# Kernel tuning notes

Hardware: AMD Instinct MI355X
Metric: run time of the kernel (lower is better)

The kernel has to match this reference:

```python
import jax, jax.numpy as jnp
import numpy as np

N = 100000
D = 64
H = 4 * D  # 256
E = 1000000


def setup_inputs() -> dict:
    key = jax.random.key(0)
    ks = jax.random.split(key, 9)
    return {
        "loc_feat": jax.random.normal(ks[0], (N, D), dtype=jnp.float32),
        "geo_src": jax.random.randint(ks[1], (E,), 0, N),
        "geo_dst": jax.random.randint(ks[2], (E,), 0, N),
        "trans_src": jax.random.randint(ks[3], (E,), 0, N),
        "trans_dst": jax.random.randint(ks[4], (E,), 0, N),
        "trans_w": jax.random.uniform(ks[5], (E,), dtype=jnp.float32),
        "W1": jax.random.normal(ks[6], (D, H), dtype=jnp.float32) * (1.0 / np.sqrt(D)),
        "b1": jax.random.normal(ks[7], (H,), dtype=jnp.float32) * 0.01,
        "W2": jax.random.normal(ks[8], (H, 1), dtype=jnp.float32) * (1.0 / np.sqrt(H)),
    }


def reference(loc_feat, geo_src, geo_dst, trans_src, trans_dst, trans_w, W1, b1, W2):
    n = loc_feat.shape[0]
    # etype 'geo': copy_u + mean  -> segment mean of src features at dst
    geo_sum = jax.ops.segment_sum(loc_feat[geo_src], geo_dst, num_segments=n)
    cnt = jax.ops.segment_sum(jnp.ones(geo_src.shape[0], loc_feat.dtype), geo_dst, num_segments=n)
    geo = jnp.where(cnt[:, None] > 0, geo_sum / jnp.maximum(cnt, 1.0)[:, None], 0.0)
    # etype 'trans': u_mul_e + sum -> weighted segment sum
    trans = jax.ops.segment_sum(loc_feat[trans_src] * trans_w[:, None], trans_dst, num_segments=n)
    # semantic attention fuse over the two relation views
    z = jnp.stack([geo, trans], axis=1)          # [N, 2, D]
    h = jnp.tanh(jnp.einsum('nkd,dh->nkh', z, W1) + b1)  # [N, 2, H]
    w = jnp.einsum('nkh,ho->nko', h, W2).mean(0)  # [2, 1] (mean over nodes)
    beta = jax.nn.softmax(w, axis=0)              # [2, 1]
    return (beta[None, :, :] * z).sum(1)          # [N, D]
```

## Files before the change

kernel.cpp:

```cpp
#include <hip/hip_runtime.h>
#include <hip/hip_bf16.h>

#define N_NODES 100000
#define DIM 64
#define HID 256
#define E_EDGES 1000000
#define TWO_N (2 * N_NODES)
#define MLP_ROWBLOCKS (TWO_N / 64)

#define TILE 240
#define NBINS 417
#define CAP 3072
#define EPB 4096
#define GEO_BLOCKS 245

typedef short short8 __attribute__((ext_vector_type(8)));
typedef float f32x4 __attribute__((ext_vector_type(4)));

__device__ __forceinline__ float tanh_fast(float x) {
    x = fminf(fmaxf(x, -15.0f), 15.0f);
    float e = __expf(2.0f * x);
    return (e - 1.0f) / (e + 1.0f);
}

__device__ __forceinline__ unsigned short f2bf(float x) {
    unsigned u = __float_as_uint(x);
    u = u + 0x7FFFu + ((u >> 16) & 1u);
    return (unsigned short)(u >> 16);
}

__global__ void bin_fill_kernel(const int* __restrict__ gs, const int* __restrict__ gd,
                                const int* __restrict__ ts, const int* __restrict__ td,
                                const float* __restrict__ tw,
                                int* __restrict__ gcount,
                                int* __restrict__ gbin, int2* __restrict__ tbin) {
    __shared__ int hist[NBINS];
    __shared__ int baseS[NBINS];
    __shared__ int cur[NBINS];
    int t = threadIdx.x;
    int blk = blockIdx.x;
    int rel = (blk >= GEO_BLOCKS) ? 1 : 0;
    int e0 = (rel ? blk - GEO_BLOCKS : blk) * EPB;
    const int* dstp = rel ? td : gd;

    for (int i = t; i < NBINS; i += 256) { hist[i] = 0; cur[i] = 0; }
    __syncthreads();

    #pragma unroll
    for (int j = 0; j < EPB / 256; ++j) {
        int e = e0 + j * 256 + t;
        if (e < E_EDGES) atomicAdd(&hist[dstp[e] / TILE], 1);
    }
    __syncthreads();

    for (int i = t; i < NBINS; i += 256) {
        int h = hist[i];
        baseS[i] = (h > 0) ? (i * CAP + atomicAdd(&gcount[rel * NBINS + i], h)) : 0;
    }
    __syncthreads();

    if (!rel) {
        #pragma unroll
        for (int j = 0; j < EPB / 256; ++j) {
            int e = e0 + j * 256 + t;
            if (e < E_EDGES) {
                int d = dstp[e];
                int bin = d / TILE;
                int pos = atomicAdd(&cur[bin], 1);
                int idx = baseS[bin] + pos;
                if (idx < (bin + 1) * CAP)
                    gbin[idx] = gs[e] | ((d - bin * TILE) << 20);
            }
        }
    } else {
        #pragma unroll
        for (int j = 0; j < EPB / 256; ++j) {
            int e = e0 + j * 256 + t;
            if (e < E_EDGES) {
                int d = dstp[e];
                int bin = d / TILE;
                int pos = atomicAdd(&cur[bin], 1);
                int idx = baseS[bin] + pos;
                if (idx < (bin + 1) * CAP)
                    tbin[idx] = make_int2(ts[e] | ((d - bin * TILE) << 20),
                                          __float_as_int(tw[e]));
            }
        }
    }
}

__global__ void __launch_bounds__(512) aggregate_kernel(
        const float* __restrict__ feat,
        const int* __restrict__ gbin, const int2* __restrict__ tbin,
        const int* __restrict__ gcount,
        float* __restrict__ out_geo, float* __restrict__ trans_out,
        int* __restrict__ cnt_out) {
    __shared__ int   srcS[CAP];
    __shared__ float wS[CAP];
    __shared__ int   histS[TILE];
    __shared__ int   baseS[TILE];
    __shared__ int   curS[TILE];
    __shared__ int   scanS[256];

    int b = blockIdx.x;
    int rel = (b >= NBINS) ? 1 : 0;
    int bin = rel ? b - NBINS : b;
    int node0 = bin * TILE;
    int nNodes = min(TILE, N_NODES - node0);
    int t = threadIdx.x, lane = t & 63, wave = t >> 6;

    int nE = gcount[b];
    if (nE > CAP) nE = CAP;

    for (int i = t; i < TILE; i += 512) histS[i] = 0;
    __syncthreads();

    if (!rel) {
        const int* bp = gbin + (size_t)bin * CAP;
        for (int i = t; i < nE; i += 512) atomicAdd(&histS[bp[i] >> 20], 1);
    } else {
        const int2* bp = tbin + (size_t)bin * CAP;
        for (int i = t; i < nE; i += 512) atomicAdd(&histS[bp[i].x >> 20], 1);
    }
    __syncthreads();

    if (t < 256) scanS[t] = (t < TILE) ? histS[t] : 0;
    __syncthreads();
    #pragma unroll
    for (int off = 1; off < 256; off <<= 1) {
        int add = 0;
        if (t < 256 && t >= off) add = scanS[t - off];
        __syncthreads();
        if (t < 256) scanS[t] += add;
        __syncthreads();
    }
    if (t < TILE) {
        int base = scanS[t] - histS[t];
        baseS[t] = base;
        curS[t] = base;
    }
    __syncthreads();

    if (!rel) {
        const int* bp = gbin + (size_t)bin * CAP;
        for (int i = t; i < nE; i += 512) {
            int p = bp[i];
            int pos = atomicAdd(&curS[p >> 20], 1);
            srcS[pos] = p & 0xFFFFF;
        }
    } else {
        const int2* bp = tbin + (size_t)bin * CAP;
        for (int i = t; i < nE; i += 512) {
            int2 p = bp[i];
            int pos = atomicAdd(&curS[p.x >> 20], 1);
            srcS[pos] = p.x & 0xFFFFF;
            wS[pos] = __int_as_float(p.y);
        }
    }
    __syncthreads();

    for (int nl = wave; nl < nNodes; nl += 8) {
        int deg = histS[nl];
        int base = baseS[nl];
        float acc = 0.0f;
        if (!rel) {
            int k = 0;
            for (; k + 3 < deg; k += 4) {
                int s0 = srcS[base + k], s1 = srcS[base + k + 1];
                int s2 = srcS[base + k + 2], s3 = srcS[base + k + 3];
                float v0 = feat[(size_t)s0 * DIM + lane];
                float v1 = feat[(size_t)s1 * DIM + lane];
                float v2 = feat[(size_t)s2 * DIM + lane];
                float v3 = feat[(size_t)s3 * DIM + lane];
                acc += (v0 + v1) + (v2 + v3);
            }
            for (; k < deg; ++k) acc += feat[(size_t)srcS[base + k] * DIM + lane];
            out_geo[(size_t)(node0 + nl) * DIM + lane] = acc;
        } else {
            int k = 0;
            for (; k + 3 < deg; k += 4) {
                int s0 = srcS[base + k], s1 = srcS[base + k + 1];
                int s2 = srcS[base + k + 2], s3 = srcS[base + k + 3];
                float w0 = wS[base + k], w1 = wS[base + k + 1];
                float w2 = wS[base + k + 2], w3 = wS[base + k + 3];
                float v0 = feat[(size_t)s0 * DIM + lane] * w0;
                float v1 = feat[(size_t)s1 * DIM + lane] * w1;
                float v2 = feat[(size_t)s2 * DIM + lane] * w2;
                float v3 = feat[(size_t)s3 * DIM + lane] * w3;
                acc += (v0 + v1) + (v2 + v3);
            }
            for (; k < deg; ++k)
                acc += feat[(size_t)srcS[base + k] * DIM + lane] * wS[base + k];
            trans_out[(size_t)(node0 + nl) * DIM + lane] = acc;
        }
    }
    if (!rel && t < nNodes) cnt_out[node0 + t] = histS[t];
}

__global__ void pack_w1_kernel(const float* __restrict__ W1, unsigned short* __restrict__ W1p) {
    int i = blockIdx.x * 256 + threadIdx.x;
    int j = i & 7;
    int r = i >> 3;
    int nidx = r & 15; r >>= 4;
    int q = r & 3; r >>= 2;
    int khalf = r & 1;
    int n = r >> 1;
    int k = 32 * khalf + 8 * q + j;
    int c = 16 * n + nidx;
    W1p[i] = f2bf(W1[k * HID + c]);
}

__global__ void __launch_bounds__(256) mlp_mfma_kernel(
        const float* __restrict__ geo_raw, const float* __restrict__ trans,
        const int* __restrict__ cnt,
        const unsigned short* __restrict__ W1p,
        const float* __restrict__ bias1, const float* __restrict__ W2,
        float* __restrict__ partials) {
    __shared__ float wred[4][2];
    int t = threadIdx.x, lane = t & 63, wave = t >> 6;
    int m = lane & 15, q = lane >> 4;
    int base = blockIdx.x * 64 + wave * 16;
    int R = base + m;

    const float* rowp;
    float scale;
    if (R < N_NODES) {
        rowp = geo_raw + (size_t)R * DIM;
        scale = 1.0f / fmaxf((float)cnt[R], 1.0f);
    } else {
        rowp = trans + (size_t)(R - N_NODES) * DIM;
        scale = 1.0f;
    }

    float4 v0 = *(const float4*)(rowp + q * 8);
    float4 v1 = *(const float4*)(rowp + q * 8 + 4);
    float4 v2 = *(const float4*)(rowp + 32 + q * 8);
    float4 v3 = *(const float4*)(rowp + 32 + q * 8 + 4);
    short8 a0, a1;
    a0[0] = (short)f2bf(v0.x * scale); a0[1] = (short)f2bf(v0.y * scale);
    a0[2] = (short)f2bf(v0.z * scale); a0[3] = (short)f2bf(v0.w * scale);
    a0[4] = (short)f2bf(v1.x * scale); a0[5] = (short)f2bf(v1.y * scale);
    a0[6] = (short)f2bf(v1.z * scale); a0[7] = (short)f2bf(v1.w * scale);
    a1[0] = (short)f2bf(v2.x * scale); a1[1] = (short)f2bf(v2.y * scale);
    a1[2] = (short)f2bf(v2.z * scale); a1[3] = (short)f2bf(v2.w * scale);
    a1[4] = (short)f2bf(v3.x * scale); a1[5] = (short)f2bf(v3.y * scale);
    a1[6] = (short)f2bf(v3.z * scale); a1[7] = (short)f2bf(v3.w * scale);

    float c0 = 0.0f, c1 = 0.0f;
    const short8* W1v = (const short8*)W1p;

    #pragma unroll 4
    for (int n = 0; n < 16; ++n) {
        short8 b0 = W1v[(n * 2 + 0) * 64 + lane];
        short8 bK = W1v[(n * 2 + 1) * 64 + lane];
        f32x4 acc = {0.0f, 0.0f, 0.0f, 0.0f};
        acc = __builtin_amdgcn_mfma_f32_16x16x32_bf16(a0, b0, acc, 0, 0, 0);
        acc = __builtin_amdgcn_mfma_f32_16x16x32_bf16(a1, bK, acc, 0, 0, 0);
        int col = 16 * n + m;
        float bj = bias1[col];
        float w2 = W2[col];
        #pragma unroll
        for (int reg = 0; reg < 4; ++reg) {
            int Rr = base + q * 4 + reg;
            float h = tanh_fast(acc[reg] + bj);
            float contrib = h * w2;
            if (Rr < N_NODES) c0 += contrib; else c1 += contrib;
        }
    }

    #pragma unroll
    for (int off = 32; off > 0; off >>= 1) {
        c0 += __shfl_down(c0, off);
        c1 += __shfl_down(c1, off);
    }
    if (lane == 0) { wred[wave][0] = c0; wred[wave][1] = c1; }
    __syncthreads();
    if (t == 0) {
        partials[blockIdx.x * 2 + 0] = wred[0][0] + wred[1][0] + wred[2][0] + wred[3][0];
        partials[blockIdx.x * 2 + 1] = wred[0][1] + wred[1][1] + wred[2][1] + wred[3][1];
    }
}

__global__ void beta_kernel(const float* __restrict__ partials, float* __restrict__ beta) {
    __shared__ float wred[4][2];
    int t = threadIdx.x;
    float c0 = 0.0f, c1 = 0.0f;
    for (int i = t; i < MLP_ROWBLOCKS; i += 256) {
        c0 += partials[i * 2 + 0];
        c1 += partials[i * 2 + 1];
    }
    #pragma unroll
    for (int off = 32; off > 0; off >>= 1) {
        c0 += __shfl_down(c0, off);
        c1 += __shfl_down(c1, off);
    }
    int lane = t & 63, wv = t >> 6;
    if (lane == 0) { wred[wv][0] = c0; wred[wv][1] = c1; }
    __syncthreads();
    if (t == 0) {
        float s0 = (wred[0][0] + wred[1][0] + wred[2][0] + wred[3][0]) / (float)N_NODES;
        float s1 = (wred[0][1] + wred[1][1] + wred[2][1] + wred[3][1]) / (float)N_NODES;
        float m = fmaxf(s0, s1);
        float e0 = __expf(s0 - m), e1 = __expf(s1 - m);
        float inv = 1.0f / (e0 + e1);
        beta[0] = e0 * inv;
        beta[1] = e1 * inv;
    }
}

__global__ void combine_kernel(float* __restrict__ out_geo,
                               const float* __restrict__ trans,
                               const int* __restrict__ cnt,
                               const float* __restrict__ beta) {
    int gid = blockIdx.x * 256 + threadIdx.x;
    int node = gid >> 4;
    float invc = 1.0f / fmaxf((float)cnt[node], 1.0f);
    float b0 = beta[0] * invc;
    float b1 = beta[1];
    float4 g = ((const float4*)out_geo)[gid];
    float4 tr = ((const float4*)trans)[gid];
    float4 o;
    o.x = b0 * g.x + b1 * tr.x;
    o.y = b0 * g.y + b1 * tr.y;
    o.z = b0 * g.z + b1 * tr.z;
    o.w = b0 * g.w + b1 * tr.w;
    ((float4*)out_geo)[gid] = o;
}

extern "C" void kernel_launch(void* const* d_in, const int* in_sizes, int n_in,
                              void* d_out, int out_size, void* d_ws, size_t ws_size,
                              hipStream_t stream) {
    const float* loc_feat = (const float*)d_in[0];
    const int* geo_src    = (const int*)d_in[1];
    const int* geo_dst    = (const int*)d_in[2];
    const int* trans_src  = (const int*)d_in[3];
    const int* trans_dst  = (const int*)d_in[4];
    const float* trans_w  = (const float*)d_in[5];
    const float* W1       = (const float*)d_in[6];
    const float* b1       = (const float*)d_in[7];
    const float* W2       = (const float*)d_in[8];
    float* out = (float*)d_out;

    float* trans    = (float*)d_ws;
    int*   cnt      = (int*)(trans + (size_t)N_NODES * DIM);
    int*   gcount   = cnt + N_NODES;
    int*   gbin     = gcount + 2 * NBINS;
    int2*  tbin     = (int2*)(gbin + (size_t)NBINS * CAP);
    float* partials = (float*)(tbin + (size_t)NBINS * CAP);
    float* beta     = partials + 2 * MLP_ROWBLOCKS;
    unsigned short* W1p = (unsigned short*)(beta + 2);

    hipMemsetAsync(gcount, 0, 2 * NBINS * sizeof(int), stream);

    pack_w1_kernel<<<64, 256, 0, stream>>>(W1, W1p);
    bin_fill_kernel<<<2 * GEO_BLOCKS, 256, 0, stream>>>(geo_src, geo_dst, trans_src,
                                                        trans_dst, trans_w,
                                                        gcount, gbin, tbin);
    aggregate_kernel<<<2 * NBINS, 512, 0, stream>>>(loc_feat, gbin, tbin, gcount,
                                                    out, trans, cnt);
    mlp_mfma_kernel<<<MLP_ROWBLOCKS, 256, 0, stream>>>(out, trans, cnt, W1p, b1, W2, partials);
    beta_kernel<<<1, 256, 0, stream>>>(partials, beta);
    combine_kernel<<<(N_NODES * DIM / 4) / 256, 256, 0, stream>>>(out, trans, cnt, beta);
}
```

Measured before the change: 261.7 us.

## Gather bf16-packed features in aggregation and vectorize edge loads in binning

Adds a pre-pass that converts node features to bf16, and the aggregation kernel now gathers 128-byte bf16 rows, processing two edges per wave with half-waves and a shuffle reduction. This halves the random gather traffic, which dominates aggregation. The binning kernel also loads dst, src and weights as int4/float4 vectors and keeps dst in registers between the histogram and scatter passes. The cost is an extra conversion kernel plus bf16 rounding of the input features, which lowers accuracy of the aggregated sums.

```diff
diff --git a/kernel.cpp b/kernel.cpp
--- a/kernel.cpp
+++ b/kernel.cpp
@@ -16,6 +16,7 @@
 
 typedef short short8 __attribute__((ext_vector_type(8)));
 typedef float f32x4 __attribute__((ext_vector_type(4)));
+typedef unsigned short us4 __attribute__((ext_vector_type(4)));
 
 __device__ __forceinline__ float tanh_fast(float x) {
     x = fminf(fmaxf(x, -15.0f), 15.0f);
@@ -27,6 +28,15 @@
     unsigned u = __float_as_uint(x);
     u = u + 0x7FFFu + ((u >> 16) & 1u);
     return (unsigned short)(u >> 16);
+}
+
+__global__ void pack_feat_kernel(const float* __restrict__ feat,
+                                 unsigned short* __restrict__ fb) {
+    int i = blockIdx.x * 256 + threadIdx.x;
+    float4 v = ((const float4*)feat)[i];
+    us4 o;
+    o[0] = f2bf(v.x); o[1] = f2bf(v.y); o[2] = f2bf(v.z); o[3] = f2bf(v.w);
+    ((us4*)fb)[i] = o;
 }
 
 __global__ void bin_fill_kernel(const int* __restrict__ gs, const int* __restrict__ gd,
@@ -42,15 +52,29 @@
     int rel = (blk >= GEO_BLOCKS) ? 1 : 0;
     int e0 = (rel ? blk - GEO_BLOCKS : blk) * EPB;
     const int* dstp = rel ? td : gd;
+    const int* srcp = rel ? ts : gs;
+
+    int dc[16];
+    #pragma unroll
+    for (int j = 0; j < 4; ++j) {
+        int idx = e0 + j * 1024 + 4 * t;
+        if (idx + 3 < E_EDGES) {
+            int4 v = *(const int4*)&dstp[idx];
+            dc[4 * j + 0] = v.x; dc[4 * j + 1] = v.y;
+            dc[4 * j + 2] = v.z; dc[4 * j + 3] = v.w;
+        } else {
+            #pragma unroll
+            for (int i2 = 0; i2 < 4; ++i2)
+                dc[4 * j + i2] = (idx + i2 < E_EDGES) ? dstp[idx + i2] : -1;
+        }
+    }
 
     for (int i = t; i < NBINS; i += 256) { hist[i] = 0; cur[i] = 0; }
     __syncthreads();
 
     #pragma unroll
-    for (int j = 0; j < EPB / 256; ++j) {
-        int e = e0 + j * 256 + t;
-        if (e < E_EDGES) atomicAdd(&hist[dstp[e] / TILE], 1);
-    }
+    for (int i = 0; i < 16; ++i)
+        if (dc[i] >= 0) atomicAdd(&hist[dc[i] / TILE], 1);
     __syncthreads();
 
     for (int i = t; i < NBINS; i += 256) {
@@ -61,36 +85,55 @@
 
     if (!rel) {
         #pragma unroll
-        for (int j = 0; j < EPB / 256; ++j) {
-            int e = e0 + j * 256 + t;
-            if (e < E_EDGES) {
-                int d = dstp[e];
+        for (int j = 0; j < 4; ++j) {
+            int idx = e0 + j * 1024 + 4 * t;
+            bool vec = (idx + 3 < E_EDGES);
+            int4 sv = {0, 0, 0, 0};
+            if (vec) sv = *(const int4*)&srcp[idx];
+            int ss[4] = {sv.x, sv.y, sv.z, sv.w};
+            #pragma unroll
+            for (int i2 = 0; i2 < 4; ++i2) {
+                int d = dc[4 * j + i2];
+                if (d < 0) continue;
+                int s = vec ? ss[i2] : srcp[idx + i2];
                 int bin = d / TILE;
                 int pos = atomicAdd(&cur[bin], 1);
-                int idx = baseS[bin] + pos;
-                if (idx < (bin + 1) * CAP)
-                    gbin[idx] = gs[e] | ((d - bin * TILE) << 20);
+                int gi = baseS[bin] + pos;
+                if (gi < (bin + 1) * CAP)
+                    gbin[gi] = s | ((d - bin * TILE) << 20);
             }
         }
     } else {
         #pragma unroll
-        for (int j = 0; j < EPB / 256; ++j) {
-            int e = e0 + j * 256 + t;
-            if (e < E_EDGES) {
-                int d = dstp[e];
+        for (int j = 0; j < 4; ++j) {
+            int idx = e0 + j * 1024 + 4 * t;
+            bool vec = (idx + 3 < E_EDGES);
+            int4 sv = {0, 0, 0, 0};
+            float4 wv = {0.f, 0.f, 0.f, 0.f};
+            if (vec) {
+                sv = *(const int4*)&srcp[idx];
+                wv = *(const float4*)&tw[idx];
+            }
+            int ss[4] = {sv.x, sv.y, sv.z, sv.w};
+            float ww[4] = {wv.x, wv.y, wv.z, wv.w};
+            #pragma unroll
+            for (int i2 = 0; i2 < 4; ++i2) {
+                int d = dc[4 * j + i2];
+                if (d < 0) continue;
+                int s = vec ? ss[i2] : srcp[idx + i2];
+                float w = vec ? ww[i2] : tw[idx + i2];
                 int bin = d / TILE;
                 int pos = atomicAdd(&cur[bin], 1);
-                int idx = baseS[bin] + pos;
-                if (idx < (bin + 1) * CAP)
-                    tbin[idx] = make_int2(ts[e] | ((d - bin * TILE) << 20),
-                                          __float_as_int(tw[e]));
+                int gi = baseS[bin] + pos;
+                if (gi < (bin + 1) * CAP)
+                    tbin[gi] = make_int2(s | ((d - bin * TILE) << 20), __float_as_int(w));
             }
         }
     }
 }
 
 __global__ void __launch_bounds__(512) aggregate_kernel(
-        const float* __restrict__ feat,
+        const unsigned short* __restrict__ featb,
         const int* __restrict__ gbin, const int2* __restrict__ tbin,
         const int* __restrict__ gcount,
         float* __restrict__ out_geo, float* __restrict__ trans_out,
@@ -108,6 +151,7 @@
     int node0 = bin * TILE;
     int nNodes = min(TILE, N_NODES - node0);
     int t = threadIdx.x, lane = t & 63, wave = t >> 6;
+    int half = lane >> 5, hl = lane & 31;
 
     int nE = gcount[b];
     if (nE > CAP) nE = CAP;
@@ -162,36 +206,76 @@
     for (int nl = wave; nl < nNodes; nl += 8) {
         int deg = histS[nl];
         int base = baseS[nl];
-        float acc = 0.0f;
+        float ax = 0.0f, ay = 0.0f;
         if (!rel) {
             int k = 0;
-            for (; k + 3 < deg; k += 4) {
-                int s0 = srcS[base + k], s1 = srcS[base + k + 1];
-                int s2 = srcS[base + k + 2], s3 = srcS[base + k + 3];
-                float v0 = feat[(size_t)s0 * DIM + lane];
-                float v1 = feat[(size_t)s1 * DIM + lane];
-                float v2 = feat[(size_t)s2 * DIM + lane];
-                float v3 = feat[(size_t)s3 * DIM + lane];
-                acc += (v0 + v1) + (v2 + v3);
-            }
-            for (; k < deg; ++k) acc += feat[(size_t)srcS[base + k] * DIM + lane];
-            out_geo[(size_t)(node0 + nl) * DIM + lane] = acc;
+            for (; k + 7 < deg; k += 8) {
+                int s0 = srcS[base + k + half];
+                int s1 = srcS[base + k + 2 + half];
+                int s2 = srcS[base + k + 4 + half];
+                int s3 = srcS[base + k + 6 + half];
+                unsigned r0 = *(const unsigned*)&featb[(size_t)s0 * DIM + 2 * hl];
+                unsigned r1 = *(const unsigned*)&featb[(size_t)s1 * DIM + 2 * hl];
+                unsigned r2 = *(const unsigned*)&featb[(size_t)s2 * DIM + 2 * hl];
+                unsigned r3 = *(const unsigned*)&featb[(size_t)s3 * DIM + 2 * hl];
+                ax += __uint_as_float(r0 << 16) + __uint_as_float(r1 << 16)
+                    + __uint_as_float(r2 << 16) + __uint_as_float(r3 << 16);
+                ay += __uint_as_float(r0 & 0xFFFF0000u) + __uint_as_float(r1 & 0xFFFF0000u)
+                    + __uint_as_float(r2 & 0xFFFF0000u) + __uint_as_float(r3 & 0xFFFF0000u);
+            }
+            for (; k + 1 < deg; k += 2) {
+                int s = srcS[base + k + half];
+                unsigned r = *(const unsigned*)&featb[(size_t)s * DIM + 2 * hl];
+                ax += __uint_as_float(r << 16);
+                ay += __uint_as_float(r & 0xFFFF0000u);
+            }
+            if (k < deg && half == 0) {
+                int s = srcS[base + k];
+                unsigned r = *(const unsigned*)&featb[(size_t)s * DIM + 2 * hl];
+                ax += __uint_as_float(r << 16);
+                ay += __uint_as_float(r & 0xFFFF0000u);
+            }
         } else {
             int k = 0;
-            for (; k + 3 < deg; k += 4) {
-                int s0 = srcS[base + k], s1 = srcS[base + k + 1];
-                int s2 = srcS[base + k + 2], s3 = srcS[base + k + 3];
-                float w0 = wS[base + k], w1 = wS[base + k + 1];
-                float w2 = wS[base + k + 2], w3 = wS[base + k + 3];
-                float v0 = feat[(size_t)s0 * DIM + lane] * w0;
-                float v1 = feat[(size_t)s1 * DIM + lane] * w1;
-                float v2 = feat[(size_t)s2 * DIM + lane] * w2;
-                float v3 = feat[(size_t)s3 * DIM + lane] * w3;
-                acc += (v0 + v1) + (v2 + v3);
-            }
-            for (; k < deg; ++k)
-                acc += feat[(size_t)srcS[base + k] * DIM + lane] * wS[base + k];
-            trans_out[(size_t)(node0 + nl) * DIM + lane] = acc;
+            for (; k + 7 < deg; k += 8) {
+                int s0 = srcS[base + k + half];
+                int s1 = srcS[base + k + 2 + half];
+                int s2 = srcS[base + k + 4 + half];
+                int s3 = srcS[base + k + 6 + half];
+                float w0 = wS[base + k + half];
+                float w1 = wS[base + k + 2 + half];
+                float w2 = wS[base + k + 4 + half];
+                float w3 = wS[base + k + 6 + half];
+                unsigned r0 = *(const unsigned*)&featb[(size_t)s0 * DIM + 2 * hl];
+                unsigned r1 = *(const unsigned*)&featb[(size_t)s1 * DIM + 2 * hl];
+                unsigned r2 = *(const unsigned*)&featb[(size_t)s2 * DIM + 2 * hl];
+                unsigned r3 = *(const unsigned*)&featb[(size_t)s3 * DIM + 2 * hl];
+                ax += __uint_as_float(r0 << 16) * w0 + __uint_as_float(r1 << 16) * w1
+                    + __uint_as_float(r2 << 16) * w2 + __uint_as_float(r3 << 16) * w3;
+                ay += __uint_as_float(r0 & 0xFFFF0000u) * w0 + __uint_as_float(r1 & 0xFFFF0000u) * w1
+                    + __uint_as_float(r2 & 0xFFFF0000u) * w2 + __uint_as_float(r3 & 0xFFFF0000u) * w3;
+            }
+            for (; k + 1 < deg; k += 2) {
+                int s = srcS[base + k + half];
+                float w = wS[base + k + half];
+                unsigned r = *(const unsigned*)&featb[(size_t)s * DIM + 2 * hl];
+                ax += __uint_as_float(r << 16) * w;
+                ay += __uint_as_float(r & 0xFFFF0000u) * w;
+            }
+            if (k < deg && half == 0) {
+                int s = srcS[base + k];
+                float w = wS[base + k];
+                unsigned r = *(const unsigned*)&featb[(size_t)s * DIM + 2 * hl];
+                ax += __uint_as_float(r << 16) * w;
+                ay += __uint_as_float(r & 0xFFFF0000u) * w;
+            }
+        }
+        ax += __shfl_down(ax, 32);
+        ay += __shfl_down(ay, 32);
+        if (half == 0) {
+            float* outp = (rel ? trans_out : out_geo) + (size_t)(node0 + nl) * DIM + 2 * hl;
+            float2 o; o.x = ax; o.y = ay;
+            *(float2*)outp = o;
         }
     }
     if (!rel && t < nNodes) cnt_out[node0 + t] = histS[t];
@@ -348,15 +432,17 @@
     int2*  tbin     = (int2*)(gbin + (size_t)NBINS * CAP);
     float* partials = (float*)(tbin + (size_t)NBINS * CAP);
     float* beta     = partials + 2 * MLP_ROWBLOCKS;
-    unsigned short* W1p = (unsigned short*)(beta + 2);
+    unsigned short* W1p   = (unsigned short*)(beta + 2);
+    unsigned short* featb = W1p + 16384;
 
     hipMemsetAsync(gcount, 0, 2 * NBINS * sizeof(int), stream);
 
+    pack_feat_kernel<<<(N_NODES * DIM / 4) / 256, 256, 0, stream>>>(loc_feat, featb);
     pack_w1_kernel<<<64, 256, 0, stream>>>(W1, W1p);
     bin_fill_kernel<<<2 * GEO_BLOCKS, 256, 0, stream>>>(geo_src, geo_dst, trans_src,
                                                         trans_dst, trans_w,
                                                         gcount, gbin, tbin);
-    aggregate_kernel<<<2 * NBINS, 512, 0, stream>>>(loc_feat, gbin, tbin, gcount,
+    aggregate_kernel<<<2 * NBINS, 512, 0, stream>>>(featb, gbin, tbin, gcount,
                                                     out, trans, cnt);
     mlp_mfma_kernel<<<MLP_ROWBLOCKS, 256, 0, stream>>>(out, trans, cnt, W1p, b1, W2, partials);
     beta_kernel<<<1, 256, 0, stream>>>(partials, beta);
```

Measured after the change: 252.0 us. 1.04x faster.
